# Performance work log

Measured on AMD Instinct MI355X. Metric: run time of the kernel, lower is better.

Reference implementation:

```python
import jax, jax.numpy as jnp
import numpy as np

B = 16384
F = 1024
DELTA = 0.3
LAMB = 0.0005


def setup_inputs() -> dict:
    key = jax.random.key(0)
    k1, k2, k3, k4 = jax.random.split(key, 4)
    skt = jax.random.normal(k1, (B, F), dtype=jnp.float32)
    imgp = jax.random.normal(k2, (B, F), dtype=jnp.float32)
    imgn = jax.random.normal(k3, (B, F), dtype=jnp.float32)
    eye = jnp.eye(F, dtype=jnp.float32)
    w = eye + 0.05 * jax.random.normal(k4, (F, F), dtype=jnp.float32)
    return {"skt": skt, "imgp": imgp, "imgn": imgn, "w": w, "eye": eye}


def _distance(v1, v2, w, w_rowsum, w_colsum):
    # sum_{i,j} w[i,j] * (v1[:,i] - v2[:,j])**2
    #   = (v1**2) @ w.sum(1) - 2 * v1 @ w @ v2^T (diag) + (v2**2) @ w.sum(0)
    cross = ((v1 @ w) * v2).sum(axis=-1)  # [B]
    return (v1 * v1) @ w_rowsum - 2.0 * cross + (v2 * v2) @ w_colsum


def reference(skt, imgp, imgn, w, eye):
    w_rowsum = w.sum(axis=1)  # [F]
    w_colsum = w.sum(axis=0)  # [F]
    dp = _distance(skt, imgp, w, w_rowsum, w_colsum)  # [B]
    dn = _distance(skt, imgn, w, w_rowsum, w_colsum)  # [B]
    hinge = jnp.maximum(DELTA + dp - dn, 0.0).mean()
    dw = w - eye
    regu = jnp.abs(dw).sum() + jnp.sqrt((dw * dw).sum())
    return hinge + LAMB * regu
```

## Files before the change

kernel.cpp:

```cpp
#include <hip/hip_runtime.h>
#include <hip/hip_bf16.h>

#define FDIM 1024
#define BROWS 16384
#define DELTA_C 0.3f
#define LAMB_C 0.0005f

typedef __bf16 bf8v __attribute__((ext_vector_type(8)));
typedef float f4v __attribute__((ext_vector_type(4)));
typedef unsigned short u16;
typedef u16 u16x8 __attribute__((ext_vector_type(8)));

#define WS_PABS_OFF 4160
#define WS_PSQ_OFF 4672
#define WS_ROWACC_OFF 8192
#define WS_WB_OFF 131072
#define WS_SKTB_OFF (131072 + (1u << 21))
#define WS_NEED_FULL ((size_t)WS_SKTB_OFF + ((size_t)1 << 25))

__device__ __forceinline__ u16 f2bf(float f) {
  unsigned u = __builtin_bit_cast(unsigned, f);
  u += 0x7fffu + ((u >> 16) & 1u);
  return (u16)(u >> 16);
}

__device__ __forceinline__ void gload_lds16(const void* g, void* l) {
  __builtin_amdgcn_global_load_lds(
      (const __attribute__((address_space(1))) unsigned int*)g,
      (__attribute__((address_space(3))) unsigned int*)l, 16, 0, 0);
}

template <bool DO_A>
__global__ __launch_bounds__(256) void prep_all(const float* __restrict__ w,
                                                const float* __restrict__ skt,
                                                float* __restrict__ colsum,
                                                float* __restrict__ pabs,
                                                float* __restrict__ psq,
                                                u16* __restrict__ wb,
                                                u16* __restrict__ sktb) {
  __shared__ char smem_u[17440];
  const int t = threadIdx.x;
  const int bid = blockIdx.x;

  if (bid < 128) {
    u16(*tile)[1024] = (u16(*)[1024])smem_u;
    float* red = (float*)(smem_u + 16384);
    const int b = bid;
    const int k0 = b * 8;
    const int col = t * 4;

    float cs0 = 0.f, cs1 = 0.f, cs2 = 0.f, cs3 = 0.f;
    float aacc = 0.f, sacc = 0.f;
#pragma unroll
    for (int i = 0; i < 8; ++i) {
      const int gk = k0 + i;
      const float4 v = *(const float4*)(w + (size_t)gk * FDIM + col);
      ushort4 bb;
      bb.x = f2bf(v.x); bb.y = f2bf(v.y); bb.z = f2bf(v.z); bb.w = f2bf(v.w);
      *(ushort4*)(&tile[i][col]) = bb;
      cs0 += v.x; cs1 += v.y; cs2 += v.z; cs3 += v.w;
      const float d0 = v.x - (gk == col + 0 ? 1.f : 0.f);
      const float d1 = v.y - (gk == col + 1 ? 1.f : 0.f);
      const float d2 = v.z - (gk == col + 2 ? 1.f : 0.f);
      const float d3 = v.w - (gk == col + 3 ? 1.f : 0.f);
      aacc += fabsf(d0) + fabsf(d1) + fabsf(d2) + fabsf(d3);
      sacc += d0 * d0 + d1 * d1 + d2 * d2 + d3 * d3;
    }
    atomicAdd(&colsum[col + 0], cs0);
    atomicAdd(&colsum[col + 1], cs1);
    atomicAdd(&colsum[col + 2], cs2);
    atomicAdd(&colsum[col + 3], cs3);
#pragma unroll
    for (int off = 1; off < 64; off <<= 1) {
      aacc += __shfl_xor(aacc, off);
      sacc += __shfl_xor(sacc, off);
    }
    const int wid = t >> 6;
    if ((t & 63) == 0) { red[wid] = aacc; red[4 + wid] = sacc; }
    __syncthreads();
    if (t == 0) pabs[b] = red[0] + red[1] + red[2] + red[3];
    if (t == 1) psq[b] = red[4] + red[5] + red[6] + red[7];
#pragma unroll
    for (int j = 0; j < 4; ++j) {
      const int n = col + j;
      u16x8 pk;
#pragma unroll
      for (int e = 0; e < 8; ++e) pk[e] = tile[e][n];
      *(u16x8*)(wb + ((size_t)b * FDIM + n) * 8) = pk;
    }
  } else if constexpr (DO_A) {
    u16(*tile)[136] = (u16(*)[136])smem_u;
    const int ab = bid - 128;
    const int mb = ab >> 3;
    const int kb = ab & 7;
    const int m0 = mb * 64, k0 = kb * 128;
#pragma unroll
    for (int i = 0; i < 8; ++i) {
      const int fid = i * 256 + t;
      const int ml = fid >> 5;
      const int c4 = fid & 31;
      const float4 v = *(const float4*)(skt + (size_t)(m0 + ml) * FDIM + k0 + c4 * 4);
      ushort4 b;
      b.x = f2bf(v.x); b.y = f2bf(v.y); b.z = f2bf(v.z); b.w = f2bf(v.w);
      *(ushort4*)(&tile[ml][c4 * 4]) = b;
    }
    __syncthreads();
    const int ks0 = k0 >> 3;
#pragma unroll
    for (int i = 0; i < 4; ++i) {
      const int uid = i * 256 + t;
      const int si = uid >> 6;
      const int ml = uid & 63;
      const u16x8 pk = *(const u16x8*)(&tile[ml][si * 8]);
      *(u16x8*)(sktb + ((size_t)(ks0 + si) * BROWS + m0 + ml) * 8) = pk;
    }
  }
}

template <bool PRE>
__global__ __launch_bounds__(512, 4) void hofel_main(
    const float* __restrict__ skt, const float* __restrict__ imgp,
    const float* __restrict__ imgn, const u16* __restrict__ wb,
    const u16* __restrict__ sktb, const float* __restrict__ colsum,
    float* __restrict__ rowacc) {
  __shared__ u16 ldsT[2][12288];
  __shared__ float lds_cs[128];

  const int t = threadIdx.x;
  const int lane = t & 63;
  const int wid = t >> 6;
  const int l15 = lane & 15;
  const int l4 = lane >> 4;

  const int swz = (blockIdx.x & 7) * 64 + (blockIdx.x >> 3);
  const int mt = swz >> 3, nt = swz & 7;
  const int m0 = mt * 256, n0 = nt * 128;

  const int wr = wid >> 1, wc = wid & 1;
  const int wm = wr * 64, wn = wc * 64;

  f4v acc[4][4];
#pragma unroll
  for (int mi = 0; mi < 4; ++mi)
#pragma unroll
    for (int ni = 0; ni < 4; ++ni) {
      f4v z = {0.f, 0.f, 0.f, 0.f};
      acc[mi][ni] = z;
    }

  auto stage = [&](int buf, int kt) {
    if constexpr (PRE) {
#pragma unroll
      for (int r = 0; r < 3; ++r) {
        const int o = r * 8192 + wid * 1024;
        const int ol = o + lane * 16;
        const char* src;
        if (ol < 16384) {
          const int s = ol >> 12;
          const int m = (ol >> 4) & 255;
          src = (const char*)(sktb + ((size_t)(kt * 4 + s) * BROWS + m0 + m) * 8);
        } else {
          const int o2 = ol - 16384;
          const int s = o2 >> 11;
          const int n = (o2 >> 4) & 127;
          src = (const char*)(wb + ((size_t)(kt * 4 + s) * FDIM + n0 + n) * 8);
        }
        gload_lds16(src, (char*)ldsT[buf] + o);
      }
    } else {
      {
        const int o = wid * 1024;
        const int ol = o + lane * 16;
        const int s = ol >> 11;
        const int n = (ol >> 4) & 127;
        gload_lds16((const char*)(wb + ((size_t)(kt * 4 + s) * FDIM + n0 + n) * 8),
                    (char*)ldsT[buf] + 16384 + o);
      }
      const int m = t >> 1, h = t & 1;
      const float* ap = skt + (size_t)(m0 + m) * FDIM + kt * 32 + h * 16;
#pragma unroll
      for (int q = 0; q < 2; ++q) {
        const float4 v0 = *(const float4*)(ap + q * 8);
        const float4 v1 = *(const float4*)(ap + q * 8 + 4);
        u16x8 pk;
        pk[0] = f2bf(v0.x); pk[1] = f2bf(v0.y); pk[2] = f2bf(v0.z); pk[3] = f2bf(v0.w);
        pk[4] = f2bf(v1.x); pk[5] = f2bf(v1.y); pk[6] = f2bf(v1.z); pk[7] = f2bf(v1.w);
        *(u16x8*)((char*)ldsT[buf] + (h * 2 + q) * 4096 + m * 16) = pk;
      }
    }
  };

  stage(0, 0);
  if (t < 128) lds_cs[t] = colsum[n0 + t];
  __syncthreads();

  int cur = 0;
  for (int kt = 0; kt < 32; ++kt) {
    if (kt < 31) stage(cur ^ 1, kt + 1);

    const char* bufb = (const char*)ldsT[cur];
    bf8v aF[4], bF[4];
#pragma unroll
    for (int mi = 0; mi < 4; ++mi)
      aF[mi] = *(const bf8v*)(bufb + l4 * 4096 + (wm + mi * 16 + l15) * 16);
#pragma unroll
    for (int ni = 0; ni < 4; ++ni)
      bF[ni] = *(const bf8v*)(bufb + 16384 + l4 * 2048 + (wn + ni * 16 + l15) * 16);
#pragma unroll
    for (int mi = 0; mi < 4; ++mi)
#pragma unroll
      for (int ni = 0; ni < 4; ++ni)
        acc[mi][ni] = __builtin_amdgcn_mfma_f32_16x16x32_bf16(aF[mi], bF[ni], acc[mi][ni], 0, 0, 0);

    __syncthreads();
    cur ^= 1;
  }

  {
    float(*eT)[68] = (float(*)[68])((char*)ldsT + wid * 4352);
    const int r = l15;
    const int qb = l4;
#pragma unroll
    for (int mi = 0; mi < 4; ++mi) {
#pragma unroll
      for (int ni = 0; ni < 4; ++ni)
#pragma unroll
        for (int rr = 0; rr < 4; ++rr)
          eT[l4 * 4 + rr][ni * 16 + l15] = acc[mi][ni][rr];
      const int rowg = m0 + wm + mi * 16 + r;
      const float* pr = imgp + (size_t)rowg * FDIM + n0 + wn;
      const float* nr = imgn + (size_t)rowg * FDIM + n0 + wn;
      float part = 0.f;
#pragma unroll
      for (int i = 0; i < 4; ++i) {
        const int q = qb + 4 * i;
        const f4v T = *(const f4v*)&eT[r][q * 4];
        const float4 p = *(const float4*)(pr + q * 4);
        const float4 n = *(const float4*)(nr + q * 4);
        const f4v cs = *(const f4v*)&lds_cs[wn + q * 4];
        part += (p.x - n.x) * (-2.f * T[0] + (p.x + n.x) * cs[0]);
        part += (p.y - n.y) * (-2.f * T[1] + (p.y + n.y) * cs[1]);
        part += (p.z - n.z) * (-2.f * T[2] + (p.z + n.z) * cs[2]);
        part += (p.w - n.w) * (-2.f * T[3] + (p.w + n.w) * cs[3]);
      }
      part += __shfl_xor(part, 16);
      part += __shfl_xor(part, 32);
      if (lane < 16) atomicAdd(rowacc + rowg, part);
      __syncthreads();
    }
  }
}

__global__ __launch_bounds__(1024) void hinge_reduce(const float* __restrict__ rowacc,
                                                     float* __restrict__ wsf) {
  __shared__ float part[16];
  const int t = threadIdx.x;
  const int id = blockIdx.x * 1024 + t;
  float v = fmaxf(DELTA_C + rowacc[id], 0.f);
#pragma unroll
  for (int off = 1; off < 64; off <<= 1) v += __shfl_xor(v, off);
  if ((t & 63) == 0) part[t >> 6] = v;
  __syncthreads();
  if (t < 16) {
    float x = part[t];
#pragma unroll
    for (int off = 1; off < 16; off <<= 1) x += __shfl_xor(x, off);
    if (t == 0) atomicAdd(&wsf[0], x);
  }
}

__global__ __launch_bounds__(128) void finalize_k(const float* __restrict__ wsf,
                                                  const float* __restrict__ pabs,
                                                  const float* __restrict__ psq,
                                                  float* __restrict__ out) {
  __shared__ float ra[2], rs[2];
  const int t = threadIdx.x;
  float a = pabs[t], s = psq[t];
#pragma unroll
  for (int off = 1; off < 64; off <<= 1) {
    a += __shfl_xor(a, off);
    s += __shfl_xor(s, off);
  }
  if ((t & 63) == 0) { ra[t >> 6] = a; rs[t >> 6] = s; }
  __syncthreads();
  if (t == 0)
    out[0] = wsf[0] * (1.f / (float)BROWS) +
             LAMB_C * ((ra[0] + ra[1]) + sqrtf(rs[0] + rs[1]));
}

extern "C" void kernel_launch(void* const* d_in, const int* in_sizes, int n_in,
                              void* d_out, int out_size, void* d_ws, size_t ws_size,
                              hipStream_t stream) {
  const float* skt  = (const float*)d_in[0];
  const float* imgp = (const float*)d_in[1];
  const float* imgn = (const float*)d_in[2];
  const float* w    = (const float*)d_in[3];

  float* wsf = (float*)d_ws;
  float* colsum = wsf + 16;
  float* pabs = (float*)((char*)d_ws + WS_PABS_OFF);
  float* psq = (float*)((char*)d_ws + WS_PSQ_OFF);
  float* rowacc = (float*)((char*)d_ws + WS_ROWACC_OFF);
  u16* wb = (u16*)((char*)d_ws + WS_WB_OFF);
  u16* sktb = (u16*)((char*)d_ws + WS_SKTB_OFF);
  float* out = (float*)d_out;

  hipMemsetAsync(d_ws, 0, WS_ROWACC_OFF + BROWS * sizeof(float), stream);

  if (ws_size >= WS_NEED_FULL) {
    prep_all<true><<<128 + 2048, 256, 0, stream>>>(w, skt, colsum, pabs, psq, wb, sktb);
    hofel_main<true><<<512, 512, 0, stream>>>(skt, imgp, imgn, wb, sktb, colsum, rowacc);
  } else {
    prep_all<false><<<128, 256, 0, stream>>>(w, skt, colsum, pabs, psq, wb, sktb);
    hofel_main<false><<<512, 512, 0, stream>>>(skt, imgp, imgn, wb, sktb, colsum, rowacc);
  }

  hinge_reduce<<<16, 1024, 0, stream>>>(rowacc, wsf);
  finalize_k<<<1, 128, 0, stream>>>(wsf, pabs, psq, out);
}
```

Baseline: 86.76 us.

## Contract on (imgp-imgn) @ w^T and drop the bf16 skt pre-pass

The distance difference is rewritten so the matmul runs on (imgp-imgn) against a transposed bf16 w, and the epilogue takes a dot product with skt. This removes the separate prep pass that converted skt to bf16 in the workspace, and the epilogue now reads one fp32 stream instead of two. The colsum quadratic term is computed in the main loop, but only by the n-tile-0 blocks. In exchange the main loop loads and converts two fp32 streams in registers each k-step, and the work per block becomes uneven.

```diff
diff --git a/kernel.cpp b/kernel.cpp
--- a/kernel.cpp
+++ b/kernel.cpp
@@ -15,8 +15,7 @@
 #define WS_PSQ_OFF 4672
 #define WS_ROWACC_OFF 8192
 #define WS_WB_OFF 131072
-#define WS_SKTB_OFF (131072 + (1u << 21))
-#define WS_NEED_FULL ((size_t)WS_SKTB_OFF + ((size_t)1 << 25))
+#define WS_NEED ((size_t)WS_WB_OFF + (1u << 21))
 
 __device__ __forceinline__ u16 f2bf(float f) {
   unsigned u = __builtin_bit_cast(unsigned, f);
@@ -30,101 +29,67 @@
       (__attribute__((address_space(3))) unsigned int*)l, 16, 0, 0);
 }
 
-template <bool DO_A>
-__global__ __launch_bounds__(256) void prep_all(const float* __restrict__ w,
-                                                const float* __restrict__ skt,
-                                                float* __restrict__ colsum,
-                                                float* __restrict__ pabs,
-                                                float* __restrict__ psq,
-                                                u16* __restrict__ wb,
-                                                u16* __restrict__ sktb) {
-  __shared__ char smem_u[17440];
+__global__ __launch_bounds__(256) void prep_w(const float* __restrict__ w,
+                                              float* __restrict__ colsum,
+                                              float* __restrict__ pabs,
+                                              float* __restrict__ psq,
+                                              u16* __restrict__ wb2) {
+  __shared__ u16 tile[8][1024];
+  __shared__ float red[8];
   const int t = threadIdx.x;
-  const int bid = blockIdx.x;
-
-  if (bid < 128) {
-    u16(*tile)[1024] = (u16(*)[1024])smem_u;
-    float* red = (float*)(smem_u + 16384);
-    const int b = bid;
-    const int k0 = b * 8;
-    const int col = t * 4;
-
-    float cs0 = 0.f, cs1 = 0.f, cs2 = 0.f, cs3 = 0.f;
-    float aacc = 0.f, sacc = 0.f;
-#pragma unroll
-    for (int i = 0; i < 8; ++i) {
-      const int gk = k0 + i;
-      const float4 v = *(const float4*)(w + (size_t)gk * FDIM + col);
-      ushort4 bb;
-      bb.x = f2bf(v.x); bb.y = f2bf(v.y); bb.z = f2bf(v.z); bb.w = f2bf(v.w);
-      *(ushort4*)(&tile[i][col]) = bb;
-      cs0 += v.x; cs1 += v.y; cs2 += v.z; cs3 += v.w;
-      const float d0 = v.x - (gk == col + 0 ? 1.f : 0.f);
-      const float d1 = v.y - (gk == col + 1 ? 1.f : 0.f);
-      const float d2 = v.z - (gk == col + 2 ? 1.f : 0.f);
-      const float d3 = v.w - (gk == col + 3 ? 1.f : 0.f);
-      aacc += fabsf(d0) + fabsf(d1) + fabsf(d2) + fabsf(d3);
-      sacc += d0 * d0 + d1 * d1 + d2 * d2 + d3 * d3;
-    }
-    atomicAdd(&colsum[col + 0], cs0);
-    atomicAdd(&colsum[col + 1], cs1);
-    atomicAdd(&colsum[col + 2], cs2);
-    atomicAdd(&colsum[col + 3], cs3);
-#pragma unroll
-    for (int off = 1; off < 64; off <<= 1) {
-      aacc += __shfl_xor(aacc, off);
-      sacc += __shfl_xor(sacc, off);
-    }
-    const int wid = t >> 6;
-    if ((t & 63) == 0) { red[wid] = aacc; red[4 + wid] = sacc; }
-    __syncthreads();
-    if (t == 0) pabs[b] = red[0] + red[1] + red[2] + red[3];
-    if (t == 1) psq[b] = red[4] + red[5] + red[6] + red[7];
-#pragma unroll
-    for (int j = 0; j < 4; ++j) {
-      const int n = col + j;
-      u16x8 pk;
-#pragma unroll
-      for (int e = 0; e < 8; ++e) pk[e] = tile[e][n];
-      *(u16x8*)(wb + ((size_t)b * FDIM + n) * 8) = pk;
-    }
-  } else if constexpr (DO_A) {
-    u16(*tile)[136] = (u16(*)[136])smem_u;
-    const int ab = bid - 128;
-    const int mb = ab >> 3;
-    const int kb = ab & 7;
-    const int m0 = mb * 64, k0 = kb * 128;
-#pragma unroll
-    for (int i = 0; i < 8; ++i) {
-      const int fid = i * 256 + t;
-      const int ml = fid >> 5;
-      const int c4 = fid & 31;
-      const float4 v = *(const float4*)(skt + (size_t)(m0 + ml) * FDIM + k0 + c4 * 4);
-      ushort4 b;
-      b.x = f2bf(v.x); b.y = f2bf(v.y); b.z = f2bf(v.z); b.w = f2bf(v.w);
-      *(ushort4*)(&tile[ml][c4 * 4]) = b;
-    }
-    __syncthreads();
-    const int ks0 = k0 >> 3;
-#pragma unroll
-    for (int i = 0; i < 4; ++i) {
-      const int uid = i * 256 + t;
-      const int si = uid >> 6;
-      const int ml = uid & 63;
-      const u16x8 pk = *(const u16x8*)(&tile[ml][si * 8]);
-      *(u16x8*)(sktb + ((size_t)(ks0 + si) * BROWS + m0 + ml) * 8) = pk;
-    }
+  const int b = blockIdx.x;
+  const int k0 = b * 8;
+  const int col = t * 4;
+
+  float cs0 = 0.f, cs1 = 0.f, cs2 = 0.f, cs3 = 0.f;
+  float aacc = 0.f, sacc = 0.f;
+#pragma unroll
+  for (int i = 0; i < 8; ++i) {
+    const int gk = k0 + i;
+    const float4 v = *(const float4*)(w + (size_t)gk * FDIM + col);
+    ushort4 bb;
+    bb.x = f2bf(v.x); bb.y = f2bf(v.y); bb.z = f2bf(v.z); bb.w = f2bf(v.w);
+    *(ushort4*)(&tile[i][col]) = bb;
+    cs0 += v.x; cs1 += v.y; cs2 += v.z; cs3 += v.w;
+    const float d0 = v.x - (gk == col + 0 ? 1.f : 0.f);
+    const float d1 = v.y - (gk == col + 1 ? 1.f : 0.f);
+    const float d2 = v.z - (gk == col + 2 ? 1.f : 0.f);
+    const float d3 = v.w - (gk == col + 3 ? 1.f : 0.f);
+    aacc += fabsf(d0) + fabsf(d1) + fabsf(d2) + fabsf(d3);
+    sacc += d0 * d0 + d1 * d1 + d2 * d2 + d3 * d3;
+  }
+  atomicAdd(&colsum[col + 0], cs0);
+  atomicAdd(&colsum[col + 1], cs1);
+  atomicAdd(&colsum[col + 2], cs2);
+  atomicAdd(&colsum[col + 3], cs3);
+#pragma unroll
+  for (int off = 1; off < 64; off <<= 1) {
+    aacc += __shfl_xor(aacc, off);
+    sacc += __shfl_xor(sacc, off);
+  }
+  const int wv = t >> 6;
+  if ((t & 63) == 0) { red[wv] = aacc; red[4 + wv] = sacc; }
+  __syncthreads();
+  if (t == 0) pabs[b] = red[0] + red[1] + red[2] + red[3];
+  if (t == 1) psq[b] = red[4] + red[5] + red[6] + red[7];
+#pragma unroll
+  for (int q = 0; q < 4; ++q) {
+    const int idx = q * 256 + t;
+    const int i = idx >> 7;
+    const int js = idx & 127;
+    const u16x8 pk = *(const u16x8*)&tile[i][js * 8];
+    *(u16x8*)(wb2 + ((size_t)js * FDIM + k0 + i) * 8) = pk;
   }
 }
 
 template <bool PRE>
 __global__ __launch_bounds__(512, 4) void hofel_main(
     const float* __restrict__ skt, const float* __restrict__ imgp,
-    const float* __restrict__ imgn, const u16* __restrict__ wb,
-    const u16* __restrict__ sktb, const float* __restrict__ colsum,
+    const float* __restrict__ imgn, const float* __restrict__ w,
+    const u16* __restrict__ wb2, const float* __restrict__ colsum,
     float* __restrict__ rowacc) {
   __shared__ u16 ldsT[2][12288];
-  __shared__ float lds_cs[128];
+  __shared__ float lds_cs[FDIM];
 
   const int t = threadIdx.x;
   const int lane = t & 63;
@@ -139,6 +104,10 @@
   const int wr = wid >> 1, wc = wid & 1;
   const int wm = wr * 64, wn = wc * 64;
 
+  const int sm = t >> 1, sh = t & 1;
+  const bool do_s2 = (nt == 0);
+  float s2 = 0.f;
+
   f4v acc[4][4];
 #pragma unroll
   for (int mi = 0; mi < 4; ++mi)
@@ -148,55 +117,75 @@
       acc[mi][ni] = z;
     }
 
-  auto stage = [&](int buf, int kt) {
+  float4 P[4], Q[4];
+
+  auto stage_load = [&](int kt) {
+    const size_t ro = (size_t)(m0 + sm) * FDIM + kt * 32 + sh * 16;
+    const float* pp = imgp + ro;
+    const float* qq = imgn + ro;
+#pragma unroll
+    for (int i = 0; i < 4; ++i) P[i] = *(const float4*)(pp + i * 4);
+#pragma unroll
+    for (int i = 0; i < 4; ++i) Q[i] = *(const float4*)(qq + i * 4);
+  };
+
+  auto stageB = [&](int buf, int kt) {
     if constexpr (PRE) {
-#pragma unroll
-      for (int r = 0; r < 3; ++r) {
-        const int o = r * 8192 + wid * 1024;
-        const int ol = o + lane * 16;
-        const char* src;
-        if (ol < 16384) {
-          const int s = ol >> 12;
-          const int m = (ol >> 4) & 255;
-          src = (const char*)(sktb + ((size_t)(kt * 4 + s) * BROWS + m0 + m) * 8);
-        } else {
-          const int o2 = ol - 16384;
-          const int s = o2 >> 11;
-          const int n = (o2 >> 4) & 127;
-          src = (const char*)(wb + ((size_t)(kt * 4 + s) * FDIM + n0 + n) * 8);
-        }
-        gload_lds16(src, (char*)ldsT[buf] + o);
+      const int o = wid * 1024;
+      const int ol = o + lane * 16;
+      const int s = ol >> 11;
+      const int n = (ol >> 4) & 127;
+      gload_lds16((const char*)(wb2 + ((size_t)(kt * 4 + s) * FDIM + n0 + n) * 8),
+                  (char*)ldsT[buf] + 16384 + o);
+    } else {
+      const int kc = t >> 2, s = t & 3;
+      const float* wr_ = w + (size_t)(n0 + kc) * FDIM + kt * 32 + s * 8;
+      const float4 a = *(const float4*)(wr_);
+      const float4 b = *(const float4*)(wr_ + 4);
+      u16x8 pk;
+      pk[0] = f2bf(a.x); pk[1] = f2bf(a.y); pk[2] = f2bf(a.z); pk[3] = f2bf(a.w);
+      pk[4] = f2bf(b.x); pk[5] = f2bf(b.y); pk[6] = f2bf(b.z); pk[7] = f2bf(b.w);
+      *(u16x8*)((char*)ldsT[buf] + 16384 + (s * 128 + kc) * 16) = pk;
+    }
+  };
+
+  auto stage_write = [&](int buf, int kt) {
+    float pn[16];
+#pragma unroll
+    for (int i = 0; i < 4; ++i) {
+      pn[i * 4 + 0] = P[i].x - Q[i].x;
+      pn[i * 4 + 1] = P[i].y - Q[i].y;
+      pn[i * 4 + 2] = P[i].z - Q[i].z;
+      pn[i * 4 + 3] = P[i].w - Q[i].w;
+    }
+    u16x8 w0, w1;
+#pragma unroll
+    for (int e = 0; e < 8; ++e) { w0[e] = f2bf(pn[e]); w1[e] = f2bf(pn[8 + e]); }
+    *(u16x8*)((char*)ldsT[buf] + (sh * 2 + 0) * 4096 + sm * 16) = w0;
+    *(u16x8*)((char*)ldsT[buf] + (sh * 2 + 1) * 4096 + sm * 16) = w1;
+    if (do_s2) {
+      const int c0 = kt * 32 + sh * 16;
+#pragma unroll
+      for (int i = 0; i < 4; ++i) {
+        const f4v cs = *(const f4v*)&lds_cs[c0 + i * 4];
+        s2 += pn[i * 4 + 0] * (P[i].x + Q[i].x) * cs[0];
+        s2 += pn[i * 4 + 1] * (P[i].y + Q[i].y) * cs[1];
+        s2 += pn[i * 4 + 2] * (P[i].z + Q[i].z) * cs[2];
+        s2 += pn[i * 4 + 3] * (P[i].w + Q[i].w) * cs[3];
       }
-    } else {
-      {
-        const int o = wid * 1024;
-        const int ol = o + lane * 16;
-        const int s = ol >> 11;
-        const int n = (ol >> 4) & 127;
-        gload_lds16((const char*)(wb + ((size_t)(kt * 4 + s) * FDIM + n0 + n) * 8),
-                    (char*)ldsT[buf] + 16384 + o);
-      }
-      const int m = t >> 1, h = t & 1;
-      const float* ap = skt + (size_t)(m0 + m) * FDIM + kt * 32 + h * 16;
-#pragma unroll
-      for (int q = 0; q < 2; ++q) {
-        const float4 v0 = *(const float4*)(ap + q * 8);
-        const float4 v1 = *(const float4*)(ap + q * 8 + 4);
-        u16x8 pk;
-        pk[0] = f2bf(v0.x); pk[1] = f2bf(v0.y); pk[2] = f2bf(v0.z); pk[3] = f2bf(v0.w);
-        pk[4] = f2bf(v1.x); pk[5] = f2bf(v1.y); pk[6] = f2bf(v1.z); pk[7] = f2bf(v1.w);
-        *(u16x8*)((char*)ldsT[buf] + (h * 2 + q) * 4096 + m * 16) = pk;
-      }
     }
   };
 
-  stage(0, 0);
-  if (t < 128) lds_cs[t] = colsum[n0 + t];
+  if (do_s2) { lds_cs[t] = colsum[t]; lds_cs[t + 512] = colsum[t + 512]; }
+  stage_load(0);
+  stageB(0, 0);
+  __syncthreads();
+  stage_write(0, 0);
   __syncthreads();
 
   int cur = 0;
   for (int kt = 0; kt < 32; ++kt) {
-    if (kt < 31) stage(cur ^ 1, kt + 1);
+    if (kt < 31) { stage_load(kt + 1); stageB(cur ^ 1, kt + 1); }
 
     const char* bufb = (const char*)ldsT[cur];
     bf8v aF[4], bF[4];
@@ -212,9 +201,12 @@
       for (int ni = 0; ni < 4; ++ni)
         acc[mi][ni] = __builtin_amdgcn_mfma_f32_16x16x32_bf16(aF[mi], bF[ni], acc[mi][ni], 0, 0, 0);
 
+    if (kt < 31) stage_write(cur ^ 1, kt + 1);
     __syncthreads();
     cur ^= 1;
   }
+
+  if (do_s2) atomicAdd(rowacc + m0 + sm, s2);
 
   {
     float(*eT)[68] = (float(*)[68])((char*)ldsT + wid * 4352);
@@ -228,25 +220,18 @@
         for (int rr = 0; rr < 4; ++rr)
           eT[l4 * 4 + rr][ni * 16 + l15] = acc[mi][ni][rr];
       const int rowg = m0 + wm + mi * 16 + r;
-      const float* pr = imgp + (size_t)rowg * FDIM + n0 + wn;
-      const float* nr = imgn + (size_t)rowg * FDIM + n0 + wn;
+      const float* sr = skt + (size_t)rowg * FDIM + n0 + wn;
       float part = 0.f;
 #pragma unroll
       for (int i = 0; i < 4; ++i) {
         const int q = qb + 4 * i;
         const f4v T = *(const f4v*)&eT[r][q * 4];
-        const float4 p = *(const float4*)(pr + q * 4);
-        const float4 n = *(const float4*)(nr + q * 4);
-        const f4v cs = *(const f4v*)&lds_cs[wn + q * 4];
-        part += (p.x - n.x) * (-2.f * T[0] + (p.x + n.x) * cs[0]);
-        part += (p.y - n.y) * (-2.f * T[1] + (p.y + n.y) * cs[1]);
-        part += (p.z - n.z) * (-2.f * T[2] + (p.z + n.z) * cs[2]);
-        part += (p.w - n.w) * (-2.f * T[3] + (p.w + n.w) * cs[3]);
+        const float4 s4 = *(const float4*)(sr + q * 4);
+        part += T[0] * s4.x + T[1] * s4.y + T[2] * s4.z + T[3] * s4.w;
       }
       part += __shfl_xor(part, 16);
       part += __shfl_xor(part, 32);
-      if (lane < 16) atomicAdd(rowacc + rowg, part);
-      __syncthreads();
+      if (lane < 16) atomicAdd(rowacc + rowg, -2.f * part);
     }
   }
 }
@@ -301,18 +286,17 @@
   float* pabs = (float*)((char*)d_ws + WS_PABS_OFF);
   float* psq = (float*)((char*)d_ws + WS_PSQ_OFF);
   float* rowacc = (float*)((char*)d_ws + WS_ROWACC_OFF);
-  u16* wb = (u16*)((char*)d_ws + WS_WB_OFF);
-  u16* sktb = (u16*)((char*)d_ws + WS_SKTB_OFF);
+  u16* wb2 = (u16*)((char*)d_ws + WS_WB_OFF);
   float* out = (float*)d_out;
 
   hipMemsetAsync(d_ws, 0, WS_ROWACC_OFF + BROWS * sizeof(float), stream);
 
-  if (ws_size >= WS_NEED_FULL) {
-    prep_all<true><<<128 + 2048, 256, 0, stream>>>(w, skt, colsum, pabs, psq, wb, sktb);
-    hofel_main<true><<<512, 512, 0, stream>>>(skt, imgp, imgn, wb, sktb, colsum, rowacc);
+  prep_w<<<128, 256, 0, stream>>>(w, colsum, pabs, psq, wb2);
+
+  if (ws_size >= WS_NEED) {
+    hofel_main<true><<<512, 512, 0, stream>>>(skt, imgp, imgn, w, wb2, colsum, rowacc);
   } else {
-    prep_all<false><<<128, 256, 0, stream>>>(w, skt, colsum, pabs, psq, wb, sktb);
-    hofel_main<false><<<512, 512, 0, stream>>>(skt, imgp, imgn, wb, sktb, colsum, rowacc);
+    hofel_main<false><<<512, 512, 0, stream>>>(skt, imgp, imgn, w, wb2, colsum, rowacc);
   }
 
   hinge_reduce<<<16, 1024, 0, stream>>>(rowacc, wsf);
```

Result: slower. 200.3 us (+130.9%).

## Replace LDS-staged GEMM with per-wave direct global fragment loads

Applied to the files above, without the earlier changes.

The main GEMM kernel stops staging A and B tiles through double-buffered LDS with global_load_lds and block barriers. Each wave now computes an independent 64x64 tile, loading MFMA fragments straight from the pre-packed bf16 buffers into registers with a two-stage register ping-pong. Block size drops to 256 threads with 1024 blocks, and colsum is read from global memory instead of LDS. This removes the barriers and LDS traffic, but gives up sharing of A/B tiles between waves, so global/L2 traffic rises and register pressure grows.

```diff
diff --git a/kernel.cpp b/kernel.cpp
--- a/kernel.cpp
+++ b/kernel.cpp
@@ -22,12 +22,6 @@
   unsigned u = __builtin_bit_cast(unsigned, f);
   u += 0x7fffu + ((u >> 16) & 1u);
   return (u16)(u >> 16);
-}
-
-__device__ __forceinline__ void gload_lds16(const void* g, void* l) {
-  __builtin_amdgcn_global_load_lds(
-      (const __attribute__((address_space(1))) unsigned int*)g,
-      (__attribute__((address_space(3))) unsigned int*)l, 16, 0, 0);
 }
 
 template <bool DO_A>
@@ -75,8 +69,8 @@
       aacc += __shfl_xor(aacc, off);
       sacc += __shfl_xor(sacc, off);
     }
-    const int wid = t >> 6;
-    if ((t & 63) == 0) { red[wid] = aacc; red[4 + wid] = sacc; }
+    const int wv = t >> 6;
+    if ((t & 63) == 0) { red[wv] = aacc; red[4 + wv] = sacc; }
     __syncthreads();
     if (t == 0) pabs[b] = red[0] + red[1] + red[2] + red[3];
     if (t == 1) psq[b] = red[4] + red[5] + red[6] + red[7];
@@ -118,13 +112,12 @@
 }
 
 template <bool PRE>
-__global__ __launch_bounds__(512, 4) void hofel_main(
+__global__ __launch_bounds__(256, 3) void hofel_main(
     const float* __restrict__ skt, const float* __restrict__ imgp,
-    const float* __restrict__ imgn, const u16* __restrict__ wb,
-    const u16* __restrict__ sktb, const float* __restrict__ colsum,
-    float* __restrict__ rowacc) {
-  __shared__ u16 ldsT[2][12288];
-  __shared__ float lds_cs[128];
+    const float* __restrict__ imgn, const float* __restrict__ w,
+    const u16* __restrict__ wb, const u16* __restrict__ sktb,
+    const float* __restrict__ colsum, float* __restrict__ rowacc) {
+  __shared__ float eT_all[4][16][68];
 
   const int t = threadIdx.x;
   const int lane = t & 63;
@@ -132,12 +125,12 @@
   const int l15 = lane & 15;
   const int l4 = lane >> 4;
 
-  const int swz = (blockIdx.x & 7) * 64 + (blockIdx.x >> 3);
-  const int mt = swz >> 3, nt = swz & 7;
-  const int m0 = mt * 256, n0 = nt * 128;
-
-  const int wr = wid >> 1, wc = wid & 1;
-  const int wm = wr * 64, wn = wc * 64;
+  const int x = blockIdx.x & 7;
+  const int b = blockIdx.x >> 3;
+  const int tid = b * 4 + wid;
+  const int mt = x * 32 + (tid >> 4);
+  const int ntw = tid & 15;
+  const int m0 = mt * 64, n0 = ntw * 64;
 
   f4v acc[4][4];
 #pragma unroll
@@ -148,78 +141,82 @@
       acc[mi][ni] = z;
     }
 
-  auto stage = [&](int buf, int kt) {
+  const u16* aBase = sktb + ((size_t)l4 * BROWS + m0 + l15) * 8;
+  const u16* bBase = wb + ((size_t)l4 * FDIM + n0 + l15) * 8;
+
+  auto load_frags = [&](int kt, bf8v& A0, bf8v& A1, bf8v& A2, bf8v& A3,
+                        bf8v& B0, bf8v& B1, bf8v& B2, bf8v& B3) {
     if constexpr (PRE) {
-#pragma unroll
-      for (int r = 0; r < 3; ++r) {
-        const int o = r * 8192 + wid * 1024;
-        const int ol = o + lane * 16;
-        const char* src;
-        if (ol < 16384) {
-          const int s = ol >> 12;
-          const int m = (ol >> 4) & 255;
-          src = (const char*)(sktb + ((size_t)(kt * 4 + s) * BROWS + m0 + m) * 8);
-        } else {
-          const int o2 = ol - 16384;
-          const int s = o2 >> 11;
-          const int n = (o2 >> 4) & 127;
-          src = (const char*)(wb + ((size_t)(kt * 4 + s) * FDIM + n0 + n) * 8);
-        }
-        gload_lds16(src, (char*)ldsT[buf] + o);
+      const u16* ap = aBase + (size_t)kt * (4u * BROWS * 8u);
+      const u16* bp = bBase + (size_t)kt * (4u * FDIM * 8u);
+      A0 = *(const bf8v*)(ap);        A1 = *(const bf8v*)(ap + 128);
+      A2 = *(const bf8v*)(ap + 256);  A3 = *(const bf8v*)(ap + 384);
+      B0 = *(const bf8v*)(bp);        B1 = *(const bf8v*)(bp + 128);
+      B2 = *(const bf8v*)(bp + 256);  B3 = *(const bf8v*)(bp + 384);
+    } else {
+      const int k0f = kt * 32 + l4 * 8;
+      bf8v* Aout[4] = {&A0, &A1, &A2, &A3};
+      bf8v* Bout[4] = {&B0, &B1, &B2, &B3};
+#pragma unroll
+      for (int mi = 0; mi < 4; ++mi) {
+        const float* p = skt + (size_t)(m0 + mi * 16 + l15) * FDIM + k0f;
+        const float4 u0 = *(const float4*)p;
+        const float4 u1 = *(const float4*)(p + 4);
+        u16x8 pk;
+        pk[0] = f2bf(u0.x); pk[1] = f2bf(u0.y); pk[2] = f2bf(u0.z); pk[3] = f2bf(u0.w);
+        pk[4] = f2bf(u1.x); pk[5] = f2bf(u1.y); pk[6] = f2bf(u1.z); pk[7] = f2bf(u1.w);
+        *Aout[mi] = __builtin_bit_cast(bf8v, pk);
       }
-    } else {
-      {
-        const int o = wid * 1024;
-        const int ol = o + lane * 16;
-        const int s = ol >> 11;
-        const int n = (ol >> 4) & 127;
-        gload_lds16((const char*)(wb + ((size_t)(kt * 4 + s) * FDIM + n0 + n) * 8),
-                    (char*)ldsT[buf] + 16384 + o);
+#pragma unroll
+      for (int ni = 0; ni < 4; ++ni) {
+        const int n = n0 + ni * 16 + l15;
+        u16x8 pk;
+#pragma unroll
+        for (int e = 0; e < 8; ++e) pk[e] = f2bf(w[(size_t)(k0f + e) * FDIM + n]);
+        *Bout[ni] = __builtin_bit_cast(bf8v, pk);
       }
-      const int m = t >> 1, h = t & 1;
-      const float* ap = skt + (size_t)(m0 + m) * FDIM + kt * 32 + h * 16;
-#pragma unroll
-      for (int q = 0; q < 2; ++q) {
-        const float4 v0 = *(const float4*)(ap + q * 8);
-        const float4 v1 = *(const float4*)(ap + q * 8 + 4);
-        u16x8 pk;
-        pk[0] = f2bf(v0.x); pk[1] = f2bf(v0.y); pk[2] = f2bf(v0.z); pk[3] = f2bf(v0.w);
-        pk[4] = f2bf(v1.x); pk[5] = f2bf(v1.y); pk[6] = f2bf(v1.z); pk[7] = f2bf(v1.w);
-        *(u16x8*)((char*)ldsT[buf] + (h * 2 + q) * 4096 + m * 16) = pk;
-      }
     }
   };
 
-  stage(0, 0);
-  if (t < 128) lds_cs[t] = colsum[n0 + t];
-  __syncthreads();
-
-  int cur = 0;
-  for (int kt = 0; kt < 32; ++kt) {
-    if (kt < 31) stage(cur ^ 1, kt + 1);
-
-    const char* bufb = (const char*)ldsT[cur];
-    bf8v aF[4], bF[4];
-#pragma unroll
-    for (int mi = 0; mi < 4; ++mi)
-      aF[mi] = *(const bf8v*)(bufb + l4 * 4096 + (wm + mi * 16 + l15) * 16);
-#pragma unroll
-    for (int ni = 0; ni < 4; ++ni)
-      bF[ni] = *(const bf8v*)(bufb + 16384 + l4 * 2048 + (wn + ni * 16 + l15) * 16);
-#pragma unroll
-    for (int mi = 0; mi < 4; ++mi)
-#pragma unroll
-      for (int ni = 0; ni < 4; ++ni)
-        acc[mi][ni] = __builtin_amdgcn_mfma_f32_16x16x32_bf16(aF[mi], bF[ni], acc[mi][ni], 0, 0, 0);
-
-    __syncthreads();
-    cur ^= 1;
-  }
+#define MMSET(A0, A1, A2, A3, B0, B1, B2, B3)                                        \
+  do {                                                                               \
+    acc[0][0] = __builtin_amdgcn_mfma_f32_16x16x32_bf16(A0, B0, acc[0][0], 0, 0, 0); \
+    acc[0][1] = __builtin_amdgcn_mfma_f32_16x16x32_bf16(A0, B1, acc[0][1], 0, 0, 0); \
+    acc[0][2] = __builtin_amdgcn_mfma_f32_16x16x32_bf16(A0, B2, acc[0][2], 0, 0, 0); \
+    acc[0][3] = __builtin_amdgcn_mfma_f32_16x16x32_bf16(A0, B3, acc[0][3], 0, 0, 0); \
+    acc[1][0] = __builtin_amdgcn_mfma_f32_16x16x32_bf16(A1, B0, acc[1][0], 0, 0, 0); \
+    acc[1][1] = __builtin_amdgcn_mfma_f32_16x16x32_bf16(A1, B1, acc[1][1], 0, 0, 0); \
+    acc[1][2] = __builtin_amdgcn_mfma_f32_16x16x32_bf16(A1, B2, acc[1][2], 0, 0, 0); \
+    acc[1][3] = __builtin_amdgcn_mfma_f32_16x16x32_bf16(A1, B3, acc[1][3], 0, 0, 0); \
+    acc[2][0] = __builtin_amdgcn_mfma_f32_16x16x32_bf16(A2, B0, acc[2][0], 0, 0, 0); \
+    acc[2][1] = __builtin_amdgcn_mfma_f32_16x16x32_bf16(A2, B1, acc[2][1], 0, 0, 0); \
+    acc[2][2] = __builtin_amdgcn_mfma_f32_16x16x32_bf16(A2, B2, acc[2][2], 0, 0, 0); \
+    acc[2][3] = __builtin_amdgcn_mfma_f32_16x16x32_bf16(A2, B3, acc[2][3], 0, 0, 0); \
+    acc[3][0] = __builtin_amdgcn_mfma_f32_16x16x32_bf16(A3, B0, acc[3][0], 0, 0, 0); \
+    acc[3][1] = __builtin_amdgcn_mfma_f32_16x16x32_bf16(A3, B1, acc[3][1], 0, 0, 0); \
+    acc[3][2] = __builtin_amdgcn_mfma_f32_16x16x32_bf16(A3, B2, acc[3][2], 0, 0, 0); \
+    acc[3][3] = __builtin_amdgcn_mfma_f32_16x16x32_bf16(A3, B3, acc[3][3], 0, 0, 0); \
+  } while (0)
 
   {
-    float(*eT)[68] = (float(*)[68])((char*)ldsT + wid * 4352);
-    const int r = l15;
-    const int qb = l4;
+    bf8v a00, a01, a02, a03, b00, b01, b02, b03;
+    bf8v a10, a11, a12, a13, b10, b11, b12, b13;
+    load_frags(0, a00, a01, a02, a03, b00, b01, b02, b03);
+#pragma unroll
+    for (int kt = 0; kt < 30; kt += 2) {
+      load_frags(kt + 1, a10, a11, a12, a13, b10, b11, b12, b13);
+      MMSET(a00, a01, a02, a03, b00, b01, b02, b03);
+      load_frags(kt + 2, a00, a01, a02, a03, b00, b01, b02, b03);
+      MMSET(a10, a11, a12, a13, b10, b11, b12, b13);
+    }
+    load_frags(31, a10, a11, a12, a13, b10, b11, b12, b13);
+    MMSET(a00, a01, a02, a03, b00, b01, b02, b03);
+    MMSET(a10, a11, a12, a13, b10, b11, b12, b13);
+  }
+#undef MMSET
+
+  {
+    float(*eT)[68] = eT_all[wid];
 #pragma unroll
     for (int mi = 0; mi < 4; ++mi) {
 #pragma unroll
@@ -227,26 +224,25 @@
 #pragma unroll
         for (int rr = 0; rr < 4; ++rr)
           eT[l4 * 4 + rr][ni * 16 + l15] = acc[mi][ni][rr];
-      const int rowg = m0 + wm + mi * 16 + r;
-      const float* pr = imgp + (size_t)rowg * FDIM + n0 + wn;
-      const float* nr = imgn + (size_t)rowg * FDIM + n0 + wn;
+      const int rowg = m0 + mi * 16 + l15;
+      const float* pr = imgp + (size_t)rowg * FDIM + n0;
+      const float* nr = imgn + (size_t)rowg * FDIM + n0;
       float part = 0.f;
 #pragma unroll
       for (int i = 0; i < 4; ++i) {
-        const int q = qb + 4 * i;
-        const f4v T = *(const f4v*)&eT[r][q * 4];
+        const int q = l4 + 4 * i;
+        const f4v T = *(const f4v*)&eT[l15][q * 4];
         const float4 p = *(const float4*)(pr + q * 4);
         const float4 n = *(const float4*)(nr + q * 4);
-        const f4v cs = *(const f4v*)&lds_cs[wn + q * 4];
-        part += (p.x - n.x) * (-2.f * T[0] + (p.x + n.x) * cs[0]);
-        part += (p.y - n.y) * (-2.f * T[1] + (p.y + n.y) * cs[1]);
-        part += (p.z - n.z) * (-2.f * T[2] + (p.z + n.z) * cs[2]);
-        part += (p.w - n.w) * (-2.f * T[3] + (p.w + n.w) * cs[3]);
+        const float4 cs = *(const float4*)(colsum + n0 + q * 4);
+        part += (p.x - n.x) * (-2.f * T[0] + (p.x + n.x) * cs.x);
+        part += (p.y - n.y) * (-2.f * T[1] + (p.y + n.y) * cs.y);
+        part += (p.z - n.z) * (-2.f * T[2] + (p.z + n.z) * cs.z);
+        part += (p.w - n.w) * (-2.f * T[3] + (p.w + n.w) * cs.w);
       }
       part += __shfl_xor(part, 16);
       part += __shfl_xor(part, 32);
       if (lane < 16) atomicAdd(rowacc + rowg, part);
-      __syncthreads();
     }
   }
 }
@@ -309,10 +305,10 @@
 
   if (ws_size >= WS_NEED_FULL) {
     prep_all<true><<<128 + 2048, 256, 0, stream>>>(w, skt, colsum, pabs, psq, wb, sktb);
-    hofel_main<true><<<512, 512, 0, stream>>>(skt, imgp, imgn, wb, sktb, colsum, rowacc);
+    hofel_main<true><<<1024, 256, 0, stream>>>(skt, imgp, imgn, w, wb, sktb, colsum, rowacc);
   } else {
     prep_all<false><<<128, 256, 0, stream>>>(w, skt, colsum, pabs, psq, wb, sktb);
-    hofel_main<false><<<512, 512, 0, stream>>>(skt, imgp, imgn, wb, sktb, colsum, rowacc);
+    hofel_main<false><<<1024, 256, 0, stream>>>(skt, imgp, imgn, w, wb, sktb, colsum, rowacc);
   }
 
   hinge_reduce<<<16, 1024, 0, stream>>>(rowacc, wsf);
```

Result: slower. 137.6 us (+58.6%).
